# Kernel tuning notes

Measured on AMD Instinct MI355X. Metric: run time of the kernel, lower is better.

The kernel has to match this reference:

```python
import jax, jax.numpy as jnp
import numpy as np
from jax.ops import segment_sum

N = 100000
E = 1600000


def gcn_conv(x, W, b, src, dst, n_nodes):
    # PyG GCNConv: linear transform, then symmetric-normalized scatter-add.
    # src/dst already include self-loops; edge weights are all ones.
    h = x @ W  # [N, out]
    deg = segment_sum(jnp.ones(src.shape[0], dtype=x.dtype), dst, num_segments=n_nodes)
    dinv = jnp.where(deg > 0, jax.lax.rsqrt(jnp.maximum(deg, 1e-12)), 0.0).astype(x.dtype)
    norm = dinv[src] * dinv[dst]  # [E]
    msg = h[src] * norm[:, None]  # gather + scale, [E, out]
    out = segment_sum(msg, dst, num_segments=n_nodes)  # scatter-add
    return out + b


def setup_inputs() -> dict:
    key = jax.random.key(0)
    k1, k2, k3, k4 = jax.random.split(key, 4)
    x = jax.random.normal(k1, (N, 128), dtype=jnp.float32)
    edge_index = jax.random.randint(k2, (2, E), 0, N, dtype=jnp.int32)
    # Glorot-ish scaled weights
    W1 = jax.random.normal(k3, (128, 64), dtype=jnp.float32) * (1.0 / np.sqrt(128))
    b1 = jnp.zeros((64,), dtype=jnp.float32)
    W2 = jax.random.normal(k4, (64, 32), dtype=jnp.float32) * (1.0 / np.sqrt(64))
    b2 = jnp.zeros((32,), dtype=jnp.float32)
    return {"x": x, "edge_index": edge_index, "W1": W1, "b1": b1, "W2": W2, "b2": b2}


def reference(x, edge_index, W1, b1, W2, b2):
    n = x.shape[0]
    # add self-loops (PyG default add_self_loops=True)
    loops = jnp.arange(n, dtype=edge_index.dtype)
    src = jnp.concatenate([edge_index[0], loops])
    dst = jnp.concatenate([edge_index[1], loops])
    h = gcn_conv(x, W1, b1, src, dst, n)
    h = jax.nn.relu(h)
    out = gcn_conv(h, W2, b2, src, dst, n)
    return out
```

## Files before the change

### kernel.cpp

```cpp
#include <hip/hip_runtime.h>
#include <hip/hip_fp16.h>

#define BS 256
#define BSHIFT 9
#define BNODES (1 << BSHIFT)
#define NBKT 256
#define CAP 12288
#define CHUNK 4096

typedef _Float16 f16x8 __attribute__((ext_vector_type(8)));
typedef float f32x4 __attribute__((ext_vector_type(4)));


__global__ __launch_bounds__(BS) void k_scatter(const int* __restrict__ src,
                                                const int* __restrict__ dst,
                                                int* __restrict__ gcursor,
                                                int* __restrict__ binned, int E) {
    __shared__ int sh[NBKT];
    __shared__ int sbase[NBKT];
    int t = threadIdx.x;
    sh[t] = 0;
    __syncthreads();
    int cbase = blockIdx.x * CHUNK;
    int sv[CHUNK / BS], dv[CHUNK / BS], rv[CHUNK / BS];
#pragma unroll
    for (int j = 0; j < CHUNK / BS; ++j) {
        int e = cbase + j * BS + t;
        rv[j] = -1;
        if (e < E) {
            sv[j] = src[e];
            dv[j] = dst[e];
            rv[j] = atomicAdd(&sh[dv[j] >> BSHIFT], 1);
        }
    }
    __syncthreads();
    sbase[t] = sh[t] ? atomicAdd(&gcursor[t], sh[t]) : 0;
    __syncthreads();
#pragma unroll
    for (int j = 0; j < CHUNK / BS; ++j) {
        if (rv[j] >= 0) {
            int b = dv[j] >> BSHIFT;
            binned[(size_t)b * CAP + sbase[b] + rv[j]] =
                sv[j] | ((dv[j] & (BNODES - 1)) << 17);
        }
    }
}


__global__ __launch_bounds__(BS) void k_build(const int* __restrict__ binned,
                                              const int* __restrict__ cnts,
                                              int2* __restrict__ rowptr2,
                                              float* __restrict__ dinv,
                                              int* __restrict__ csr, int n) {
    __shared__ int h[BNODES];
    __shared__ int rp[BNODES];
    __shared__ int cur[BNODES];
    __shared__ int ws[4];
    int t = threadIdx.x;
    int bkt = blockIdx.x;
    int node0 = bkt << BSHIFT;
    int nn = min(BNODES, n - node0);
#pragma unroll
    for (int i = t; i < BNODES; i += BS) h[i] = 0;
    __syncthreads();
    int cnt = cnts[bkt];
    const int* eb = binned + (size_t)bkt * CAP;
    for (int e = t; e < cnt; e += BS) atomicAdd(&h[eb[e] >> 17], 1);
    __syncthreads();
    int i0 = 2 * t;
    int v0 = h[i0], v1 = h[i0 + 1];
    int pair = v0 + v1;
    int lane = t & 63, w = t >> 6;
    int incl = pair;
#pragma unroll
    for (int off = 1; off < 64; off <<= 1) {
        int u = __shfl_up(incl, off);
        if (lane >= off) incl += u;
    }
    if (lane == 63) ws[w] = incl;
    __syncthreads();
    int woff = 0;
    for (int q = 0; q < w; ++q) woff += ws[q];
    int excl = woff + incl - pair;
    int cb = bkt * (CAP + BNODES);
    int r0 = cb + excl + i0;
    int r1 = r0 + v0 + 1;
    rp[i0] = r0; rp[i0 + 1] = r1;
    cur[i0] = 1; cur[i0 + 1] = 1;
    if (i0 < nn) {
        rowptr2[node0 + i0] = make_int2(r0, r1);
        dinv[node0 + i0] = rsqrtf((float)(v0 + 1));
        csr[r0] = node0 + i0;
    }
    if (i0 + 1 < nn) {
        rowptr2[node0 + i0 + 1] = make_int2(r1, r1 + v1 + 1);
        dinv[node0 + i0 + 1] = rsqrtf((float)(v1 + 1));
        csr[r1] = node0 + i0 + 1;
    }
    __syncthreads();
    for (int e = t; e < cnt; e += BS) {
        int p = eb[e];
        int li = p >> 17;
        int r = atomicAdd(&cur[li], 1);
        csr[rp[li] + r] = p & 0x1FFFF;
    }
}


__global__ __launch_bounds__(BS, 4) void k_mgemm1(const float* __restrict__ X,
                                                  const float* __restrict__ W,
                                                  const float* __restrict__ dscale,
                                                  __half* __restrict__ H, int n) {
    constexpr int K = 128, COLS = 64;
    constexpr int KC = K / 8;
    constexpr int SWZ = 15;
    constexpr int NT = COLS / 16;
    __shared__ __align__(16) _Float16 sB[COLS * K];
    int tid = threadIdx.x;
    for (int idx = tid; idx < COLS * KC; idx += BS) {
        int c = idx / KC, k8 = idx % KC;
        f16x8 v;
#pragma unroll
        for (int j = 0; j < 8; ++j) v[j] = (_Float16)W[(k8 * 8 + j) * COLS + c];
        *(f16x8*)&sB[c * K + ((k8 ^ (c & SWZ)) * 8)] = v;
    }
    __syncthreads();
    int w = tid >> 6, lane = tid & 63;
    int lm = lane & 15, q = lane >> 4;
    int row_m0 = blockIdx.x * 128 + w * 32;
    f32x4 acc[2][NT];
#pragma unroll
    for (int tm = 0; tm < 2; ++tm)
#pragma unroll
        for (int tn = 0; tn < NT; ++tn) acc[tm][tn] = (f32x4){0.f, 0.f, 0.f, 0.f};
#pragma unroll
    for (int kk = 0; kk < K / 32; ++kk) {
        int k0 = kk * 32 + q * 8;
        f16x8 af[2], bf[NT];
#pragma unroll
        for (int tm = 0; tm < 2; ++tm) {
            int row = row_m0 + tm * 16 + lm;
            int rl = row < n ? row : (n - 1);
            const float4* xp = (const float4*)X + ((size_t)rl * K + k0) / 4;
            float4 a = xp[0], b = xp[1];
            f16x8 v;
            v[0] = (_Float16)a.x; v[1] = (_Float16)a.y;
            v[2] = (_Float16)a.z; v[3] = (_Float16)a.w;
            v[4] = (_Float16)b.x; v[5] = (_Float16)b.y;
            v[6] = (_Float16)b.z; v[7] = (_Float16)b.w;
            af[tm] = v;
        }
#pragma unroll
        for (int tn = 0; tn < NT; ++tn) {
            int c = tn * 16 + lm;
            bf[tn] = *(const f16x8*)&sB[c * K + (((kk * 4 + q) ^ (c & SWZ)) * 8)];
        }
#pragma unroll
        for (int tm = 0; tm < 2; ++tm)
#pragma unroll
            for (int tn = 0; tn < NT; ++tn)
                acc[tm][tn] = __builtin_amdgcn_mfma_f32_16x16x32_f16(af[tm], bf[tn],
                                                                     acc[tm][tn], 0, 0, 0);
    }
#pragma unroll
    for (int tm = 0; tm < 2; ++tm) {
#pragma unroll
        for (int r = 0; r < 4; ++r) {
            int row = row_m0 + tm * 16 + q * 4 + r;
            if (row < n) {
                float dv = dscale[row];
#pragma unroll
                for (int tn = 0; tn < NT; ++tn) {
                    int col = tn * 16 + lm;
                    H[(size_t)row * COLS + col] = __float2half_rn(acc[tm][tn][r] * dv);
                }
            }
        }
    }
}


__device__ __forceinline__ void acc_pk(float4 raw, __half2& p0, __half2& p1,
                                       __half2& p2, __half2& p3) {
    const __half2* u = (const __half2*)&raw;
    p0 = __hadd2(p0, u[0]); p1 = __hadd2(p1, u[1]);
    p2 = __hadd2(p2, u[2]); p3 = __hadd2(p3, u[3]);
}

__global__ __launch_bounds__(BS) void k_aggmm(const __half* __restrict__ h,
                                              const int* __restrict__ csr,
                                              const int2* __restrict__ rowptr2,
                                              const float* __restrict__ dinv,
                                              const float* __restrict__ b1,
                                              const float* __restrict__ W2,
                                              __half* __restrict__ h2, int n) {
    __shared__ float sW2[64 * 32];
    __shared__ float sB1[64];
    __shared__ float sU[(BS / 64) * 2 * 64];
    int t = threadIdx.x;
    for (int i = t; i < 64 * 32; i += BS) sW2[i] = W2[i];
    if (t < 64) sB1[t] = b1[t];
    __syncthreads();

    int npairs = (n + 1) / 2;
    int wib = t >> 6;
    int wid = blockIdx.x * (BS / 64) + wib;
    if (wid >= npairs) return;
    int lane = t & 63;
    int half = lane >> 5, hl = lane & 31;
    int node = wid * 2 + half;
    bool valid = node < n;
    int b = 0, e = 0;
    if (valid) { int2 be = rowptr2[node]; b = be.x; e = be.y; }
    int slot = hl >> 3, fq = hl & 7;
    __half2 pA0 = __float2half2_rn(0.f), pA1 = pA0, pA2 = pA0, pA3 = pA0;
    __half2 pB0 = pA0, pB1 = pA0, pB2 = pA0, pB3 = pA0;
    for (int c = b; c < e; c += 32) {
        int m = e - c;
        if (m > 32) m = 32;
        int sv = (hl < m) ? csr[c + hl] : 0;
        int j = 0;
        for (; j + 7 < m; j += 8) {
            int s0 = __shfl(sv, j + slot, 32);
            int s1 = __shfl(sv, j + 4 + slot, 32);
            float4 r0 = *((const float4*)(h + (size_t)s0 * 64) + fq);
            float4 r1 = *((const float4*)(h + (size_t)s1 * 64) + fq);
            acc_pk(r0, pA0, pA1, pA2, pA3);
            acc_pk(r1, pB0, pB1, pB2, pB3);
        }
        for (; j < m; j += 4) {
            int js = j + slot;
            int s = __shfl(sv, js < m ? js : 0, 32);
            if (js < m) {
                float4 r0 = *((const float4*)(h + (size_t)s * 64) + fq);
                acc_pk(r0, pA0, pA1, pA2, pA3);
            }
        }
    }
    float2 f0 = __half22float2(pA0), f1 = __half22float2(pA1);
    float2 f2 = __half22float2(pA2), f3 = __half22float2(pA3);
    float2 g0 = __half22float2(pB0), g1v = __half22float2(pB1);
    float2 g2 = __half22float2(pB2), g3 = __half22float2(pB3);
    float a0 = f0.x + g0.x, a1 = f0.y + g0.y, a2 = f1.x + g1v.x, a3 = f1.y + g1v.y;
    float a4 = f2.x + g2.x, a5 = f2.y + g2.y, a6 = f3.x + g3.x, a7 = f3.y + g3.y;
    a0 += __shfl_down(a0, 16); a1 += __shfl_down(a1, 16);
    a2 += __shfl_down(a2, 16); a3 += __shfl_down(a3, 16);
    a4 += __shfl_down(a4, 16); a5 += __shfl_down(a5, 16);
    a6 += __shfl_down(a6, 16); a7 += __shfl_down(a7, 16);
    a0 += __shfl_down(a0, 8);  a1 += __shfl_down(a1, 8);
    a2 += __shfl_down(a2, 8);  a3 += __shfl_down(a3, 8);
    a4 += __shfl_down(a4, 8);  a5 += __shfl_down(a5, 8);
    a6 += __shfl_down(a6, 8);  a7 += __shfl_down(a7, 8);

    if (valid && hl < 8) {
        float dv = dinv[node];
        float* up = &sU[(wib * 2 + half) * 64 + hl * 8];
        up[0] = fmaxf(a0 * dv + sB1[hl * 8 + 0], 0.f);
        up[1] = fmaxf(a1 * dv + sB1[hl * 8 + 1], 0.f);
        up[2] = fmaxf(a2 * dv + sB1[hl * 8 + 2], 0.f);
        up[3] = fmaxf(a3 * dv + sB1[hl * 8 + 3], 0.f);
        up[4] = fmaxf(a4 * dv + sB1[hl * 8 + 4], 0.f);
        up[5] = fmaxf(a5 * dv + sB1[hl * 8 + 5], 0.f);
        up[6] = fmaxf(a6 * dv + sB1[hl * 8 + 6], 0.f);
        up[7] = fmaxf(a7 * dv + sB1[hl * 8 + 7], 0.f);
    }
    int nodeSel = lane >> 5;
    int mvnode = wid * 2 + nodeSel;
    if (mvnode < n) {
        const float* u = &sU[(wib * 2 + nodeSel) * 64];
        int cc = lane & 31;
        float acc = 0.f;
#pragma unroll
        for (int k = 0; k < 64; ++k) acc = fmaf(u[k], sW2[k * 32 + cc], acc);
        h2[(size_t)mvnode * 32 + cc] = __float2half_rn(acc * dinv[mvnode]);
    }
}


__global__ __launch_bounds__(BS) void k_agg32(const __half* __restrict__ h,
                                              const int* __restrict__ csr,
                                              const int2* __restrict__ rowptr2,
                                              const float* __restrict__ dinv,
                                              const float* __restrict__ bias,
                                              float* __restrict__ out, int n) {
    int wid = (blockIdx.x * BS + threadIdx.x) >> 6;
    int lane = threadIdx.x & 63;
    int half = lane >> 5, hl = lane & 31;
    int node = wid * 2 + half;
    bool valid = node < n;
    int b = 0, e = 0;
    if (valid) { int2 be = rowptr2[node]; b = be.x; e = be.y; }
    int slot = hl >> 2, fq = hl & 3;
    float a0 = 0.f, a1 = 0.f, a2 = 0.f, a3 = 0.f;
    float a4 = 0.f, a5 = 0.f, a6 = 0.f, a7 = 0.f;
    for (int c = b; c < e; c += 32) {
        int m = e - c;
        if (m > 32) m = 32;
        int sv = (hl < m) ? csr[c + hl] : 0;
        int j = 0;
        for (; j + 15 < m; j += 16) {
            int s0 = __shfl(sv, j + slot, 32);
            int s1 = __shfl(sv, j + 8 + slot, 32);
            float4 r0 = *((const float4*)(h + (size_t)s0 * 32) + fq);
            float4 r1 = *((const float4*)(h + (size_t)s1 * 32) + fq);
            const __half2* u0 = (const __half2*)&r0;
            const __half2* u1 = (const __half2*)&r1;
            float2 q0 = __half22float2(u0[0]), q1 = __half22float2(u0[1]);
            float2 q2 = __half22float2(u0[2]), q3 = __half22float2(u0[3]);
            a0 += q0.x; a1 += q0.y; a2 += q1.x; a3 += q1.y;
            a4 += q2.x; a5 += q2.y; a6 += q3.x; a7 += q3.y;
            q0 = __half22float2(u1[0]); q1 = __half22float2(u1[1]);
            q2 = __half22float2(u1[2]); q3 = __half22float2(u1[3]);
            a0 += q0.x; a1 += q0.y; a2 += q1.x; a3 += q1.y;
            a4 += q2.x; a5 += q2.y; a6 += q3.x; a7 += q3.y;
        }
        for (; j < m; j += 8) {
            int js = j + slot;
            int s = __shfl(sv, js < m ? js : 0, 32);
            if (js < m) {
                float4 r0 = *((const float4*)(h + (size_t)s * 32) + fq);
                const __half2* u0 = (const __half2*)&r0;
                float2 q0 = __half22float2(u0[0]), q1 = __half22float2(u0[1]);
                float2 q2 = __half22float2(u0[2]), q3 = __half22float2(u0[3]);
                a0 += q0.x; a1 += q0.y; a2 += q1.x; a3 += q1.y;
                a4 += q2.x; a5 += q2.y; a6 += q3.x; a7 += q3.y;
            }
        }
    }
    a0 += __shfl_down(a0, 16); a1 += __shfl_down(a1, 16);
    a2 += __shfl_down(a2, 16); a3 += __shfl_down(a3, 16);
    a4 += __shfl_down(a4, 16); a5 += __shfl_down(a5, 16);
    a6 += __shfl_down(a6, 16); a7 += __shfl_down(a7, 16);
    a0 += __shfl_down(a0, 8);  a1 += __shfl_down(a1, 8);
    a2 += __shfl_down(a2, 8);  a3 += __shfl_down(a3, 8);
    a4 += __shfl_down(a4, 8);  a5 += __shfl_down(a5, 8);
    a6 += __shfl_down(a6, 8);  a7 += __shfl_down(a7, 8);
    a0 += __shfl_down(a0, 4);  a1 += __shfl_down(a1, 4);
    a2 += __shfl_down(a2, 4);  a3 += __shfl_down(a3, 4);
    a4 += __shfl_down(a4, 4);  a5 += __shfl_down(a5, 4);
    a6 += __shfl_down(a6, 4);  a7 += __shfl_down(a7, 4);
    if (valid && hl < 4) {
        float dv = dinv[node];
        const float4* bp = (const float4*)bias + hl * 2;
        float4 b0 = bp[0], b1v = bp[1];
        float4 o0 = make_float4(a0 * dv + b0.x, a1 * dv + b0.y,
                                a2 * dv + b0.z, a3 * dv + b0.w);
        float4 o1 = make_float4(a4 * dv + b1v.x, a5 * dv + b1v.y,
                                a6 * dv + b1v.z, a7 * dv + b1v.w);
        float4* op = (float4*)(out + (size_t)node * 32 + hl * 8);
        op[0] = o0; op[1] = o1;
    }
}


extern "C" void kernel_launch(void* const* d_in, const int* in_sizes, int n_in,
                              void* d_out, int out_size, void* d_ws, size_t ws_size,
                              hipStream_t stream) {
    const float* x  = (const float*)d_in[0];
    const int* eidx = (const int*)d_in[1];
    const float* W1 = (const float*)d_in[2];
    const float* b1 = (const float*)d_in[3];
    const float* W2 = (const float*)d_in[4];
    const float* b2 = (const float*)d_in[5];
    float* out = (float*)d_out;

    int n = in_sizes[0] / 128;
    int E = in_sizes[1] / 2;
    const int* srcA = eidx;
    const int* dstA = eidx + E;

    char* p = (char*)d_ws;
    auto alloc = [&](size_t bytes) {
        char* q = p;
        p += (bytes + 255) & ~(size_t)255;
        return q;
    };
    int2*   rowptr2 = (int2*)alloc((size_t)n * 8);
    float*  dinv    = (float*)alloc((size_t)n * 4);
    int*    gcursor = (int*)alloc(NBKT * 4);
    int*    binned  = (int*)alloc((size_t)NBKT * CAP * 4);
    int*    csr     = (int*)alloc((size_t)NBKT * (CAP + BNODES) * 4);
    __half* h1      = (__half*)alloc((size_t)n * 64 * 2);
    __half* h2      = (__half*)alloc((size_t)n * 32 * 2);

    int nchunks  = (E + CHUNK - 1) / CHUNK;
    int nbuckets = (n + BNODES - 1) / BNODES;
    int nblk     = (n + 127) / 128;
    int npairs   = (n + 1) / 2;
    int aggblk   = (npairs + (BS / 64) - 1) / (BS / 64);

    hipMemsetAsync(gcursor, 0, NBKT * 4, stream);
    k_scatter<<<nchunks, BS, 0, stream>>>(srcA, dstA, gcursor, binned, E);
    k_build<<<nbuckets, BS, 0, stream>>>(binned, gcursor, rowptr2, dinv, csr, n);
    k_mgemm1<<<nblk, BS, 0, stream>>>(x, W1, dinv, h1, n);
    k_aggmm<<<aggblk, BS, 0, stream>>>(h1, csr, rowptr2, dinv, b1, W2, h2, n);
    k_agg32<<<aggblk, BS, 0, stream>>>(h2, csr, rowptr2, dinv, b2, out, n);
}
```

Baseline: 235.4 us.

## Fuse edge scatter and first GEMM into one launch, apply source norm in aggregation

```diff
diff --git a/kernel.cpp b/kernel.cpp
--- a/kernel.cpp
+++ b/kernel.cpp
@@ -12,36 +12,108 @@
 typedef float f32x4 __attribute__((ext_vector_type(4)));
 
 
-__global__ __launch_bounds__(BS) void k_scatter(const int* __restrict__ src,
-                                                const int* __restrict__ dst,
-                                                int* __restrict__ gcursor,
-                                                int* __restrict__ binned, int E) {
+__global__ __launch_bounds__(BS) void k_prep(const int* __restrict__ src,
+                                             const int* __restrict__ dst,
+                                             int* __restrict__ gcursor,
+                                             int* __restrict__ binned, int E,
+                                             const float* __restrict__ X,
+                                             const float* __restrict__ W,
+                                             __half* __restrict__ H, int n,
+                                             int nchunks) {
     __shared__ int sh[NBKT];
     __shared__ int sbase[NBKT];
+    __shared__ __align__(16) _Float16 sB[64 * 128];
     int t = threadIdx.x;
-    sh[t] = 0;
-    __syncthreads();
-    int cbase = blockIdx.x * CHUNK;
-    int sv[CHUNK / BS], dv[CHUNK / BS], rv[CHUNK / BS];
-#pragma unroll
-    for (int j = 0; j < CHUNK / BS; ++j) {
-        int e = cbase + j * BS + t;
-        rv[j] = -1;
-        if (e < E) {
-            sv[j] = src[e];
-            dv[j] = dst[e];
-            rv[j] = atomicAdd(&sh[dv[j] >> BSHIFT], 1);
-        }
-    }
-    __syncthreads();
-    sbase[t] = sh[t] ? atomicAdd(&gcursor[t], sh[t]) : 0;
-    __syncthreads();
-#pragma unroll
-    for (int j = 0; j < CHUNK / BS; ++j) {
-        if (rv[j] >= 0) {
-            int b = dv[j] >> BSHIFT;
-            binned[(size_t)b * CAP + sbase[b] + rv[j]] =
-                sv[j] | ((dv[j] & (BNODES - 1)) << 17);
+    if (blockIdx.x < nchunks) {
+        sh[t] = 0;
+        __syncthreads();
+        int cbase = blockIdx.x * CHUNK;
+        int sv[CHUNK / BS], dv[CHUNK / BS], rv[CHUNK / BS];
+#pragma unroll
+        for (int j = 0; j < CHUNK / BS; ++j) {
+            int e = cbase + j * BS + t;
+            rv[j] = -1;
+            if (e < E) {
+                sv[j] = src[e];
+                dv[j] = dst[e];
+                rv[j] = atomicAdd(&sh[dv[j] >> BSHIFT], 1);
+            }
+        }
+        __syncthreads();
+        sbase[t] = sh[t] ? atomicAdd(&gcursor[t], sh[t]) : 0;
+        __syncthreads();
+#pragma unroll
+        for (int j = 0; j < CHUNK / BS; ++j) {
+            if (rv[j] >= 0) {
+                int b = dv[j] >> BSHIFT;
+                binned[(size_t)b * CAP + sbase[b] + rv[j]] =
+                    sv[j] | ((dv[j] & (BNODES - 1)) << 17);
+            }
+        }
+        return;
+    }
+    constexpr int K = 128, COLS = 64;
+    constexpr int KC = K / 8;
+    constexpr int SWZ = 15;
+    constexpr int NT = COLS / 16;
+    int bid = blockIdx.x - nchunks;
+    for (int idx = t; idx < COLS * KC; idx += BS) {
+        int c = idx / KC, k8 = idx % KC;
+        f16x8 v;
+#pragma unroll
+        for (int j = 0; j < 8; ++j) v[j] = (_Float16)W[(k8 * 8 + j) * COLS + c];
+        *(f16x8*)&sB[c * K + ((k8 ^ (c & SWZ)) * 8)] = v;
+    }
+    __syncthreads();
+    int w = t >> 6, lane = t & 63;
+    int lm = lane & 15, q = lane >> 4;
+    int row_m0 = bid * 128 + w * 32;
+    f32x4 acc[2][NT];
+#pragma unroll
+    for (int tm = 0; tm < 2; ++tm)
+#pragma unroll
+        for (int tn = 0; tn < NT; ++tn) acc[tm][tn] = (f32x4){0.f, 0.f, 0.f, 0.f};
+#pragma unroll
+    for (int kk = 0; kk < K / 32; ++kk) {
+        int k0 = kk * 32 + q * 8;
+        f16x8 af[2], bf[NT];
+#pragma unroll
+        for (int tm = 0; tm < 2; ++tm) {
+            int row = row_m0 + tm * 16 + lm;
+            int rl = row < n ? row : (n - 1);
+            const float4* xp = (const float4*)X + ((size_t)rl * K + k0) / 4;
+            float4 a = xp[0], b = xp[1];
+            f16x8 v;
+            v[0] = (_Float16)a.x; v[1] = (_Float16)a.y;
+            v[2] = (_Float16)a.z; v[3] = (_Float16)a.w;
+            v[4] = (_Float16)b.x; v[5] = (_Float16)b.y;
+            v[6] = (_Float16)b.z; v[7] = (_Float16)b.w;
+            af[tm] = v;
+        }
+#pragma unroll
+        for (int tn = 0; tn < NT; ++tn) {
+            int c = tn * 16 + lm;
+            bf[tn] = *(const f16x8*)&sB[c * K + (((kk * 4 + q) ^ (c & SWZ)) * 8)];
+        }
+#pragma unroll
+        for (int tm = 0; tm < 2; ++tm)
+#pragma unroll
+            for (int tn = 0; tn < NT; ++tn)
+                acc[tm][tn] = __builtin_amdgcn_mfma_f32_16x16x32_f16(af[tm], bf[tn],
+                                                                     acc[tm][tn], 0, 0, 0);
+    }
+#pragma unroll
+    for (int tm = 0; tm < 2; ++tm) {
+#pragma unroll
+        for (int r = 0; r < 4; ++r) {
+            int row = row_m0 + tm * 16 + q * 4 + r;
+            if (row < n) {
+#pragma unroll
+                for (int tn = 0; tn < NT; ++tn) {
+                    int col = tn * 16 + lm;
+                    H[(size_t)row * COLS + col] = __float2half_rn(acc[tm][tn][r]);
+                }
+            }
         }
     }
 }
@@ -107,87 +179,14 @@
 }
 
 
-__global__ __launch_bounds__(BS, 4) void k_mgemm1(const float* __restrict__ X,
-                                                  const float* __restrict__ W,
-                                                  const float* __restrict__ dscale,
-                                                  __half* __restrict__ H, int n) {
-    constexpr int K = 128, COLS = 64;
-    constexpr int KC = K / 8;
-    constexpr int SWZ = 15;
-    constexpr int NT = COLS / 16;
-    __shared__ __align__(16) _Float16 sB[COLS * K];
-    int tid = threadIdx.x;
-    for (int idx = tid; idx < COLS * KC; idx += BS) {
-        int c = idx / KC, k8 = idx % KC;
-        f16x8 v;
-#pragma unroll
-        for (int j = 0; j < 8; ++j) v[j] = (_Float16)W[(k8 * 8 + j) * COLS + c];
-        *(f16x8*)&sB[c * K + ((k8 ^ (c & SWZ)) * 8)] = v;
-    }
-    __syncthreads();
-    int w = tid >> 6, lane = tid & 63;
-    int lm = lane & 15, q = lane >> 4;
-    int row_m0 = blockIdx.x * 128 + w * 32;
-    f32x4 acc[2][NT];
-#pragma unroll
-    for (int tm = 0; tm < 2; ++tm)
-#pragma unroll
-        for (int tn = 0; tn < NT; ++tn) acc[tm][tn] = (f32x4){0.f, 0.f, 0.f, 0.f};
-#pragma unroll
-    for (int kk = 0; kk < K / 32; ++kk) {
-        int k0 = kk * 32 + q * 8;
-        f16x8 af[2], bf[NT];
-#pragma unroll
-        for (int tm = 0; tm < 2; ++tm) {
-            int row = row_m0 + tm * 16 + lm;
-            int rl = row < n ? row : (n - 1);
-            const float4* xp = (const float4*)X + ((size_t)rl * K + k0) / 4;
-            float4 a = xp[0], b = xp[1];
-            f16x8 v;
-            v[0] = (_Float16)a.x; v[1] = (_Float16)a.y;
-            v[2] = (_Float16)a.z; v[3] = (_Float16)a.w;
-            v[4] = (_Float16)b.x; v[5] = (_Float16)b.y;
-            v[6] = (_Float16)b.z; v[7] = (_Float16)b.w;
-            af[tm] = v;
-        }
-#pragma unroll
-        for (int tn = 0; tn < NT; ++tn) {
-            int c = tn * 16 + lm;
-            bf[tn] = *(const f16x8*)&sB[c * K + (((kk * 4 + q) ^ (c & SWZ)) * 8)];
-        }
-#pragma unroll
-        for (int tm = 0; tm < 2; ++tm)
-#pragma unroll
-            for (int tn = 0; tn < NT; ++tn)
-                acc[tm][tn] = __builtin_amdgcn_mfma_f32_16x16x32_f16(af[tm], bf[tn],
-                                                                     acc[tm][tn], 0, 0, 0);
-    }
-#pragma unroll
-    for (int tm = 0; tm < 2; ++tm) {
-#pragma unroll
-        for (int r = 0; r < 4; ++r) {
-            int row = row_m0 + tm * 16 + q * 4 + r;
-            if (row < n) {
-                float dv = dscale[row];
-#pragma unroll
-                for (int tn = 0; tn < NT; ++tn) {
-                    int col = tn * 16 + lm;
-                    H[(size_t)row * COLS + col] = __float2half_rn(acc[tm][tn][r] * dv);
-                }
-            }
-        }
-    }
-}
-
-
-__device__ __forceinline__ void acc_pk(float4 raw, __half2& p0, __half2& p1,
-                                       __half2& p2, __half2& p3) {
+__device__ __forceinline__ void acc_fma(float4 raw, __half2 d, __half2& p0, __half2& p1,
+                                        __half2& p2, __half2& p3) {
     const __half2* u = (const __half2*)&raw;
-    p0 = __hadd2(p0, u[0]); p1 = __hadd2(p1, u[1]);
-    p2 = __hadd2(p2, u[2]); p3 = __hadd2(p3, u[3]);
-}
-
-__global__ __launch_bounds__(BS) void k_aggmm(const __half* __restrict__ h,
+    p0 = __hfma2(u[0], d, p0); p1 = __hfma2(u[1], d, p1);
+    p2 = __hfma2(u[2], d, p2); p3 = __hfma2(u[3], d, p3);
+}
+
+__global__ __launch_bounds__(BS) void k_aggmm(const __half* __restrict__ hsrc,
                                               const int* __restrict__ csr,
                                               const int2* __restrict__ rowptr2,
                                               const float* __restrict__ dinv,
@@ -219,21 +218,25 @@
         int m = e - c;
         if (m > 32) m = 32;
         int sv = (hl < m) ? csr[c + hl] : 0;
+        float dsv = dinv[sv];
         int j = 0;
         for (; j + 7 < m; j += 8) {
             int s0 = __shfl(sv, j + slot, 32);
+            float d0 = __shfl(dsv, j + slot, 32);
             int s1 = __shfl(sv, j + 4 + slot, 32);
-            float4 r0 = *((const float4*)(h + (size_t)s0 * 64) + fq);
-            float4 r1 = *((const float4*)(h + (size_t)s1 * 64) + fq);
-            acc_pk(r0, pA0, pA1, pA2, pA3);
-            acc_pk(r1, pB0, pB1, pB2, pB3);
+            float d1 = __shfl(dsv, j + 4 + slot, 32);
+            float4 r0 = *((const float4*)(hsrc + (size_t)s0 * 64) + fq);
+            float4 r1 = *((const float4*)(hsrc + (size_t)s1 * 64) + fq);
+            acc_fma(r0, __float2half2_rn(d0), pA0, pA1, pA2, pA3);
+            acc_fma(r1, __float2half2_rn(d1), pB0, pB1, pB2, pB3);
         }
         for (; j < m; j += 4) {
             int js = j + slot;
             int s = __shfl(sv, js < m ? js : 0, 32);
+            float d = __shfl(dsv, js < m ? js : 0, 32);
             if (js < m) {
-                float4 r0 = *((const float4*)(h + (size_t)s * 64) + fq);
-                acc_pk(r0, pA0, pA1, pA2, pA3);
+                float4 r0 = *((const float4*)(hsrc + (size_t)s * 64) + fq);
+                acc_fma(r0, __float2half2_rn(d), pA0, pA1, pA2, pA3);
             }
         }
     }
@@ -390,9 +393,9 @@
     int aggblk   = (npairs + (BS / 64) - 1) / (BS / 64);
 
     hipMemsetAsync(gcursor, 0, NBKT * 4, stream);
-    k_scatter<<<nchunks, BS, 0, stream>>>(srcA, dstA, gcursor, binned, E);
+    k_prep<<<nchunks + nblk, BS, 0, stream>>>(srcA, dstA, gcursor, binned, E,
+                                              x, W1, h1, n, nchunks);
     k_build<<<nbuckets, BS, 0, stream>>>(binned, gcursor, rowptr2, dinv, csr, n);
-    k_mgemm1<<<nblk, BS, 0, stream>>>(x, W1, dinv, h1, n);
     k_aggmm<<<aggblk, BS, 0, stream>>>(h1, csr, rowptr2, dinv, b1, W2, h2, n);
     k_agg32<<<aggblk, BS, 0, stream>>>(h2, csr, rowptr2, dinv, b2, out, n);
 }
```

Result: faster. 223.9 us (-4.9%).
